# Kernel optimization log

Hardware: AMD Instinct MI355X
Metric: run time of the kernel (lower is better)

Reference implementation:

```python
import jax, jax.numpy as jnp
import numpy as np

N_SPK = 2048   # number of speakers
U = 32         # utterances per speaker (half enrollment, half test)
D = 256        # embedding dim
EPS = 1e-8     # F.cosine_similarity eps (norm clamp)


def setup_inputs() -> dict:
    key = jax.random.key(0)
    k1, = jax.random.split(key, 1)
    embeddings = jax.random.normal(k1, (N_SPK * U, D), dtype=jnp.float32)
    labels = jnp.repeat(jnp.arange(N_SPK, dtype=jnp.int64), U)
    alpha = jnp.float32(10.0)
    beta = jnp.float32(-5.0)
    return {"embeddings": embeddings, "labels": labels, "alpha": alpha, "beta": beta}


def _ge2e_loss(embeddings, labels_np, alpha, beta):
    # labels_np: host numpy int labels (constant). Balanced: each speaker has U utts.
    n_spk = int(labels_np.max()) + 1
    u = labels_np.shape[0] // n_spk
    order = np.argsort(labels_np, kind="stable")  # group by speaker, preserve order
    emb = embeddings[order].reshape(n_spk, u, -1)           # [N, U, D]
    half = u // 2
    enroll, test = emb[:, :half], emb[:, half:]             # [N, U/2, D]
    cent = enroll.mean(axis=1)                              # [N, D]
    tn = test / jnp.maximum(jnp.linalg.norm(test, axis=-1, keepdims=True), EPS)
    cn = cent / jnp.maximum(jnp.linalg.norm(cent, axis=-1, keepdims=True), EPS)
    # cosine sim of every test utt (speaker m, utt t) vs every centroid n
    sims = alpha * jnp.einsum("mtd,nd->mtn", tn, cn) + beta  # [N, U/2, N]
    e = jnp.exp(sims)
    total = e.sum(axis=(0, 1))                               # [N] sum over all test utts per centroid
    idx = jnp.arange(n_spk)
    pos_sum = e[idx, :, idx].sum(axis=1)                     # [N] own-speaker test utts
    neg_sum = total - pos_sum                                # sum over other speakers' test utts
    loss = jnp.mean(jnp.log(neg_sum) - jnp.log(pos_sum))
    return loss


def reference(embeddings, labels, alpha, beta):
    labels_np = np.asarray(labels)
    return _ge2e_loss(embeddings, labels_np, alpha, beta)
```

## Files before the change

kernel.cpp:

```cpp
#include <hip/hip_runtime.h>
#include <hip/hip_bf16.h>
#include <stdint.h>

#define N_SPK 2048
#define UU 32
#define DD 256
#define HALF_U 16
#define M_ROWS (N_SPK * HALF_U)

#define BM 256
#define BN 256
#define BK 64

typedef __attribute__((ext_vector_type(8))) short short8;
typedef __attribute__((ext_vector_type(4))) float f32x4;

typedef const __attribute__((address_space(1))) void ga_void;
typedef __attribute__((address_space(3))) void ls_void;

__device__ __forceinline__ void gld16(const void* g, void* l) {
    __builtin_amdgcn_global_load_lds((ga_void*)(uintptr_t)g,
                                     (ls_void*)(uintptr_t)l, 16, 0, 0);
}

__device__ __forceinline__ unsigned short f2bf(float x) {
    union { float f; unsigned u; } c; c.f = x;
    unsigned r = c.u + 0x7fffu + ((c.u >> 16) & 1u);
    return (unsigned short)(r >> 16);
}

#define WAITVM(n) do { \
    asm volatile("s_waitcnt vmcnt(" #n ")" ::: "memory"); \
    __builtin_amdgcn_sched_barrier(0); \
} while (0)

#define WAITLGKM0 do { \
    asm volatile("s_waitcnt lgkmcnt(0)" ::: "memory"); \
    __builtin_amdgcn_sched_barrier(0); \
} while (0)

__global__ __launch_bounds__(256) void prep_kernel(const float* __restrict__ emb,
                                                   unsigned short* __restrict__ tn,
                                                   unsigned short* __restrict__ cn,
                                                   float* __restrict__ zbuf)
{
    if (blockIdx.x == 0) {
        #pragma unroll
        for (int i = 0; i < 16; ++i) zbuf[threadIdx.x + 256 * i] = 0.0f;
    }

    const int w = threadIdx.x >> 6;
    const int l = threadIdx.x & 63;
    const int task = blockIdx.x * 4 + w;

    float4 v;
    if (task < M_ROWS) {
        const int m = task >> 4;
        const int t = task & 15;
        const size_t grow = (size_t)m * UU + HALF_U + t;
        v = *(const float4*)(emb + grow * DD + 4 * l);
    } else {
        const int n = task - M_ROWS;
        float ax = 0.f, ay = 0.f, az = 0.f, aw = 0.f;
        const float* base = emb + (size_t)n * UU * DD + 4 * l;
        #pragma unroll
        for (int j = 0; j < HALF_U; ++j) {
            float4 e = *(const float4*)(base + j * DD);
            ax += e.x; ay += e.y; az += e.z; aw += e.w;
        }
        const float inv = 1.0f / 16.0f;
        v = make_float4(ax * inv, ay * inv, az * inv, aw * inv);
    }
    float ss = v.x * v.x + v.y * v.y + v.z * v.z + v.w * v.w;
    #pragma unroll
    for (int d = 1; d < 64; d <<= 1) ss += __shfl_xor(ss, d);
    const float sc = 1.0f / fmaxf(sqrtf(ss), 1e-8f);

    ushort4 o;
    o.x = f2bf(v.x * sc); o.y = f2bf(v.y * sc);
    o.z = f2bf(v.z * sc); o.w = f2bf(v.w * sc);
    unsigned short* dst = (task < M_ROWS)
        ? (tn + (size_t)task * DD + 4 * l)
        : (cn + (size_t)(task - M_ROWS) * DD + 4 * l);
    *(ushort4*)dst = o;
}

__global__ __launch_bounds__(512, 2) void gemm_kernel(const unsigned short* __restrict__ tnb,
                                                      const unsigned short* __restrict__ cnb,
                                                      const float* __restrict__ alphaP,
                                                      const float* __restrict__ betaP,
                                                      float* __restrict__ total,
                                                      float* __restrict__ pos)
{
    __shared__ __align__(16) char S[4][32768];
    __shared__ float csum[BN];

    const int tid = threadIdx.x;
    const int l = tid & 63;
    const int w = tid >> 6;
    const int wr = w >> 2, wc = w & 3;
    const int r16 = l & 15, hi = l >> 4;

    const float alpha = *alphaP;
    const float beta  = *betaP;

    const int c = blockIdx.x;
    const int xcd = c & 7, slot = c >> 3;
    const int bm = xcd * 16 + (slot >> 1);
    const int bn0 = (slot & 1) * 4;

    const char* gA = (const char*)tnb + (size_t)bm * BM * 512;

    auto stage_half = [&](int jj, int h) {
        const int kt = jj & 3;
        const int bn = bn0 + (jj >> 2);
        char* slotp = S[(2 * jj + h) & 3];
        const char* gB = (const char*)cnb + (size_t)bn * BN * 512;
        #pragma unroll
        for (int i = 0; i < 2; ++i) {
            const int off = i * 8192 + tid * 16;
            const int row = off >> 7;
            const int sc  = ((off >> 4) & 7) ^ (row & 7);
            const int goff = (h * 128 + row) * 512 + kt * 128 + sc * 16;
            gld16(gA + goff, slotp + off);
            gld16(gB + goff, slotp + 16384 + off);
        }
    };

    f32x4 acc[8][4] = {};

    stage_half(0, 0); stage_half(0, 1);
    stage_half(1, 0); stage_half(1, 1);
    WAITVM(8);
    __builtin_amdgcn_s_barrier();

    for (int j = 0; j < 16; ++j) {
        const char* As = S[(2 * j + wr) & 3];
        const char* Bs = S[(2 * j + (wc >> 1)) & 3] + 16384;
        short8 b[4][2];
        #pragma unroll
        for (int p = 0; p < 4; ++p) {
            short8 a[2][2];
            if (p == 0) {
                #pragma unroll
                for (int ni = 0; ni < 4; ++ni)
                    #pragma unroll
                    for (int kk = 0; kk < 2; ++kk) {
                        const int row = wc * 64 + ni * 16 + r16;
                        const int c16 = (kk * 4 + hi) ^ (row & 7);
                        b[ni][kk] = *(const short8*)(Bs + (row & 127) * 128 + c16 * 16);
                    }
            }
            #pragma unroll
            for (int m2 = 0; m2 < 2; ++m2)
                #pragma unroll
                for (int kk = 0; kk < 2; ++kk) {
                    const int mi = p * 2 + m2;
                    const int lrow = mi * 16 + r16;
                    const int c16 = (kk * 4 + hi) ^ (lrow & 7);
                    a[m2][kk] = *(const short8*)(As + lrow * 128 + c16 * 16);
                }
            if (j < 15) {
                if (p == 0) stage_half(j + 1, 0);
                if (p == 1) stage_half(j + 1, 1);
            }
            __builtin_amdgcn_s_barrier();
            WAITLGKM0;
            __builtin_amdgcn_s_setprio(1);
            #pragma unroll
            for (int kk = 0; kk < 2; ++kk)
                #pragma unroll
                for (int m2 = 0; m2 < 2; ++m2)
                    #pragma unroll
                    for (int ni = 0; ni < 4; ++ni)
                        acc[p * 2 + m2][ni] = __builtin_amdgcn_mfma_f32_16x16x32_bf16(
                            a[m2][kk], b[ni][kk], acc[p * 2 + m2][ni], 0, 0, 0);
            __builtin_amdgcn_s_setprio(0);
            __builtin_amdgcn_s_barrier();
        }

        if ((j & 3) == 3) {
            const int bn = bn0 + (j >> 2);
            const bool diag = ((bm >> 4) == bn);
            if (tid < BN) csum[tid] = 0.0f;
            __builtin_amdgcn_s_barrier();
            #pragma unroll
            for (int ni = 0; ni < 4; ++ni) {
                const int colg = bn * BN + wc * 64 + ni * 16 + r16;
                float cs = 0.f;
                #pragma unroll
                for (int mi = 0; mi < 8; ++mi) {
                    const int rowbase = bm * BM + wr * 128 + mi * 16 + hi * 4;
                    #pragma unroll
                    for (int r = 0; r < 4; ++r) {
                        const float e = __expf(alpha * acc[mi][ni][r] + beta);
                        cs += e;
                        if (diag && ((rowbase + r) >> 4) == colg)
                            atomicAdd(pos + colg, e);
                    }
                    acc[mi][ni] = (f32x4){0.f, 0.f, 0.f, 0.f};
                }
                cs += __shfl_xor(cs, 16);
                cs += __shfl_xor(cs, 32);
                if (hi == 0) atomicAdd(&csum[wc * 64 + ni * 16 + r16], cs);
            }
            __builtin_amdgcn_s_barrier();
            if (tid < BN) atomicAdd(total + bn * BN + tid, csum[tid]);
            __builtin_amdgcn_s_barrier();
        }

        if (j < 15) {
            WAITVM(0);
            __builtin_amdgcn_s_barrier();
        }
    }
}

__global__ __launch_bounds__(256) void finalize_kernel(const float* __restrict__ total,
                                                       const float* __restrict__ pos,
                                                       float* __restrict__ out)
{
    const int tid = threadIdx.x;
    float s = 0.f;
    for (int i = tid; i < N_SPK; i += 256) {
        const float p = pos[i];
        const float t = total[i];
        s += logf(t - p) - logf(p);
    }
    #pragma unroll
    for (int d = 1; d < 64; d <<= 1) s += __shfl_xor(s, d);
    __shared__ float wsum[4];
    if ((tid & 63) == 0) wsum[tid >> 6] = s;
    __syncthreads();
    if (tid == 0) out[0] = (wsum[0] + wsum[1] + wsum[2] + wsum[3]) * (1.0f / (float)N_SPK);
}

extern "C" void kernel_launch(void* const* d_in, const int* in_sizes, int n_in,
                              void* d_out, int out_size, void* d_ws, size_t ws_size,
                              hipStream_t stream)
{
    const float* emb    = (const float*)d_in[0];
    const float* alphaP = (const float*)d_in[2];
    const float* betaP  = (const float*)d_in[3];
    float* out = (float*)d_out;

    char* ws = (char*)d_ws;
    unsigned short* tn = (unsigned short*)ws;
    unsigned short* cn = (unsigned short*)(ws + 16777216);
    float* total       = (float*)(ws + 16777216 + 1048576);
    float* pos         = total + N_SPK;

    hipLaunchKernelGGL(prep_kernel, dim3((M_ROWS + N_SPK) / 4), dim3(256), 0, stream,
                       emb, tn, cn, total );
    hipLaunchKernelGGL(gemm_kernel, dim3(256), dim3(512), 0, stream,
                       tn, cn, alphaP, betaP, total, pos);
    hipLaunchKernelGGL(finalize_kernel, dim3(1), dim3(256), 0, stream,
                       total, pos, out);
}
```

Baseline: 155.9 us.

## Shrink N tile to 128 and deepen to triple-buffered two-ahead prefetch

The GEMM block tile goes from 256x256 to 256x128, and the warp layout becomes 4x2 with four accumulator rows per warp, roughly halving accumulator registers. LDS staging becomes a 9-slot ring with three 16KB units per k-step, prefetched two steps ahead, and waits on vmcnt(6) instead of draining everything each step. The goal is to hide global load latency better and relieve register pressure. In exchange each block does more B loads per unit of compute, and the epilogue reductions and atomics run twice as often.

```diff
diff --git a/kernel.cpp b/kernel.cpp
--- a/kernel.cpp
+++ b/kernel.cpp
@@ -9,8 +9,9 @@
 #define M_ROWS (N_SPK * HALF_U)
 
 #define BM 256
-#define BN 256
+#define BN 128
 #define BK 64
+#define NSTEP 32
 
 typedef __attribute__((ext_vector_type(8))) short short8;
 typedef __attribute__((ext_vector_type(4))) float f32x4;
@@ -92,13 +93,13 @@
                                                       float* __restrict__ total,
                                                       float* __restrict__ pos)
 {
-    __shared__ __align__(16) char S[4][32768];
+    __shared__ __align__(16) char S[9][16384];
     __shared__ float csum[BN];
 
     const int tid = threadIdx.x;
     const int l = tid & 63;
     const int w = tid >> 6;
-    const int wr = w >> 2, wc = w & 3;
+    const int wr = w >> 1, wc = w & 1;
     const int r16 = l & 15, hi = l >> 4;
 
     const float alpha = *alphaP;
@@ -107,63 +108,59 @@
     const int c = blockIdx.x;
     const int xcd = c & 7, slot = c >> 3;
     const int bm = xcd * 16 + (slot >> 1);
-    const int bn0 = (slot & 1) * 4;
-
-    const char* gA = (const char*)tnb + (size_t)bm * BM * 512;
-
-    auto stage_half = [&](int jj, int h) {
+    const int bn0 = (slot & 1) * 8;
+
+    const char* gA  = (const char*)tnb + (size_t)bm * BM * 512;
+    const char* gBb = (const char*)cnb;
+
+    auto stage_unit = [&](int jj, int u, int ss) {
         const int kt = jj & 3;
-        const int bn = bn0 + (jj >> 2);
-        char* slotp = S[(2 * jj + h) & 3];
-        const char* gB = (const char*)cnb + (size_t)bn * BN * 512;
+        char* dst = S[ss];
+        const char* g = (u < 2) ? gA : gBb;
+        const int rbase = (u < 2) ? u * 128 : (bn0 + (jj >> 2)) * 128;
         #pragma unroll
         for (int i = 0; i < 2; ++i) {
             const int off = i * 8192 + tid * 16;
             const int row = off >> 7;
             const int sc  = ((off >> 4) & 7) ^ (row & 7);
-            const int goff = (h * 128 + row) * 512 + kt * 128 + sc * 16;
-            gld16(gA + goff, slotp + off);
-            gld16(gB + goff, slotp + 16384 + off);
+            gld16(g + (size_t)(rbase + row) * 512 + kt * 128 + sc * 16, dst + off);
         }
     };
 
-    f32x4 acc[8][4] = {};
-
-    stage_half(0, 0); stage_half(0, 1);
-    stage_half(1, 0); stage_half(1, 1);
-    WAITVM(8);
+    f32x4 acc[4][4] = {};
+
+    #pragma unroll
+    for (int u = 0; u < 3; ++u) stage_unit(0, u, u);
+    #pragma unroll
+    for (int u = 0; u < 3; ++u) stage_unit(1, u, 3 + u);
+    WAITVM(6);
     __builtin_amdgcn_s_barrier();
 
-    for (int j = 0; j < 16; ++j) {
-        const char* As = S[(2 * j + wr) & 3];
-        const char* Bs = S[(2 * j + (wc >> 1)) & 3] + 16384;
+    int s0 = 0;
+    for (int j = 0; j < NSTEP; ++j) {
+        const int s2 = (s0 >= 3) ? s0 - 3 : s0 + 6;
+        const char* As = S[s0 + (wr >> 1)];
+        const char* Bs = S[s0 + 2];
+        const int lrA = (wr & 1) * 64;
+        const int c16k0 = hi ^ (r16 & 7);
+        const int c16k1 = (4 + hi) ^ (r16 & 7);
         short8 b[4][2];
-        #pragma unroll
-        for (int p = 0; p < 4; ++p) {
+
+        {
+            #pragma unroll
+            for (int ni = 0; ni < 4; ++ni) {
+                const int row = wc * 64 + ni * 16 + r16;
+                b[ni][0] = *(const short8*)(Bs + row * 128 + c16k0 * 16);
+                b[ni][1] = *(const short8*)(Bs + row * 128 + c16k1 * 16);
+            }
             short8 a[2][2];
-            if (p == 0) {
-                #pragma unroll
-                for (int ni = 0; ni < 4; ++ni)
-                    #pragma unroll
-                    for (int kk = 0; kk < 2; ++kk) {
-                        const int row = wc * 64 + ni * 16 + r16;
-                        const int c16 = (kk * 4 + hi) ^ (row & 7);
-                        b[ni][kk] = *(const short8*)(Bs + (row & 127) * 128 + c16 * 16);
-                    }
-            }
-            #pragma unroll
-            for (int m2 = 0; m2 < 2; ++m2)
-                #pragma unroll
-                for (int kk = 0; kk < 2; ++kk) {
-                    const int mi = p * 2 + m2;
-                    const int lrow = mi * 16 + r16;
-                    const int c16 = (kk * 4 + hi) ^ (lrow & 7);
-                    a[m2][kk] = *(const short8*)(As + lrow * 128 + c16 * 16);
-                }
-            if (j < 15) {
-                if (p == 0) stage_half(j + 1, 0);
-                if (p == 1) stage_half(j + 1, 1);
-            }
+            #pragma unroll
+            for (int m2 = 0; m2 < 2; ++m2) {
+                const int row = lrA + m2 * 16 + r16;
+                a[m2][0] = *(const short8*)(As + row * 128 + c16k0 * 16);
+                a[m2][1] = *(const short8*)(As + row * 128 + c16k1 * 16);
+            }
+            if (j < NSTEP - 2) { stage_unit(j + 2, 0, s2); stage_unit(j + 2, 1, s2 + 1); }
             __builtin_amdgcn_s_barrier();
             WAITLGKM0;
             __builtin_amdgcn_s_setprio(1);
@@ -173,15 +170,39 @@
                 for (int m2 = 0; m2 < 2; ++m2)
                     #pragma unroll
                     for (int ni = 0; ni < 4; ++ni)
-                        acc[p * 2 + m2][ni] = __builtin_amdgcn_mfma_f32_16x16x32_bf16(
-                            a[m2][kk], b[ni][kk], acc[p * 2 + m2][ni], 0, 0, 0);
+                        acc[m2][ni] = __builtin_amdgcn_mfma_f32_16x16x32_bf16(
+                            a[m2][kk], b[ni][kk], acc[m2][ni], 0, 0, 0);
+            __builtin_amdgcn_s_setprio(0);
+            __builtin_amdgcn_s_barrier();
+        }
+
+        {
+            short8 a[2][2];
+            #pragma unroll
+            for (int m2 = 0; m2 < 2; ++m2) {
+                const int row = lrA + (2 + m2) * 16 + r16;
+                a[m2][0] = *(const short8*)(As + row * 128 + c16k0 * 16);
+                a[m2][1] = *(const short8*)(As + row * 128 + c16k1 * 16);
+            }
+            if (j < NSTEP - 2) stage_unit(j + 2, 2, s2 + 2);
+            __builtin_amdgcn_s_barrier();
+            WAITLGKM0;
+            __builtin_amdgcn_s_setprio(1);
+            #pragma unroll
+            for (int kk = 0; kk < 2; ++kk)
+                #pragma unroll
+                for (int m2 = 0; m2 < 2; ++m2)
+                    #pragma unroll
+                    for (int ni = 0; ni < 4; ++ni)
+                        acc[2 + m2][ni] = __builtin_amdgcn_mfma_f32_16x16x32_bf16(
+                            a[m2][kk], b[ni][kk], acc[2 + m2][ni], 0, 0, 0);
             __builtin_amdgcn_s_setprio(0);
             __builtin_amdgcn_s_barrier();
         }
 
         if ((j & 3) == 3) {
             const int bn = bn0 + (j >> 2);
-            const bool diag = ((bm >> 4) == bn);
+            const bool diag = ((bm >> 3) == bn);
             if (tid < BN) csum[tid] = 0.0f;
             __builtin_amdgcn_s_barrier();
             #pragma unroll
@@ -189,8 +210,8 @@
                 const int colg = bn * BN + wc * 64 + ni * 16 + r16;
                 float cs = 0.f;
                 #pragma unroll
-                for (int mi = 0; mi < 8; ++mi) {
-                    const int rowbase = bm * BM + wr * 128 + mi * 16 + hi * 4;
+                for (int mi = 0; mi < 4; ++mi) {
+                    const int rowbase = bm * BM + wr * 64 + mi * 16 + hi * 4;
                     #pragma unroll
                     for (int r = 0; r < 4; ++r) {
                         const float e = __expf(alpha * acc[mi][ni][r] + beta);
@@ -206,13 +227,14 @@
             }
             __builtin_amdgcn_s_barrier();
             if (tid < BN) atomicAdd(total + bn * BN + tid, csum[tid]);
-            __builtin_amdgcn_s_barrier();
-        }
-
-        if (j < 15) {
-            WAITVM(0);
-            __builtin_amdgcn_s_barrier();
-        }
+        }
+
+        if (j < NSTEP - 1) {
+            if (j < NSTEP - 2) { WAITVM(6); }
+            else               { WAITVM(0); }
+            __builtin_amdgcn_s_barrier();
+        }
+        s0 = (s0 >= 6) ? 0 : s0 + 3;
     }
 }
 
```

New measurement: 164.7 us. 5.6% more time.
